# Performance work log

Measured on AMD Instinct MI355X. Metric: run time of the kernel, lower is better.

Reference implementation:

```python
import jax, jax.numpy as jnp
import numpy as np

CHUNK = 32
H = 4

def silu(x):
    return x * jax.nn.sigmoid(x)

def l2norm(x):
    return x * jax.lax.rsqrt(jnp.sum(x * x, -1, keepdims=True) + 1e-6)

def dwconv_causal(x_cl, w):
    # x_cl: (b, C, L), w: (C, k) depthwise causal conv (cross-correlation, left pad k-1)
    k = w.shape[1]
    xp = jnp.pad(x_cl, ((0, 0), (0, 0), (k - 1, 0)))
    return jax.lax.conv_general_dilated(xp, w[:, None, :], (1,), 'VALID',
        dimension_numbers=('NCH', 'OIH', 'NCH'), feature_group_count=x_cl.shape[1])

def short_conv_silu(x_bld, w):
    y = dwconv_causal(jnp.swapaxes(x_bld, 1, 2), w)
    return silu(jnp.swapaxes(y, 1, 2))

def delta_rule_chunkwise(q, k, v, beta, chunk=CHUNK):
    # q,k: (b,h,L,dk)  v: (b,h,L,dv)  beta: (b,h,L)
    b, h, L, dk = q.shape
    dv = v.shape[-1]
    pad = (-L) % chunk
    if pad:
        q, k, v = (jnp.pad(t, ((0, 0), (0, 0), (0, pad), (0, 0))) for t in (q, k, v))
        beta = jnp.pad(beta, ((0, 0), (0, 0), (0, pad)))
    n = (L + pad) // chunk
    q = l2norm(q)
    k = l2norm(k)
    v = v * beta[..., None]
    kb = k * beta[..., None]
    ch = lambda x: x.reshape(b, h, n, chunk, x.shape[-1])
    qc, kc, vc, kbc = map(ch, (q, k, v, kb))
    idx = jnp.arange(chunk)
    strict_lower = (idx[:, None] > idx[None, :]).astype(q.dtype)
    incl_lower = (idx[:, None] >= idx[None, :]).astype(q.dtype)
    # forward substitution to invert (I - tril(beta K K^T, -1)) per chunk
    attn = -jnp.einsum('bhncd,bhned->bhnce', kbc, kc) * strict_lower
    for i in range(1, chunk):
        upd = jnp.einsum('...j,...ji->...i', attn[..., i, :], attn[..., :, :i])
        attn = attn.at[..., i, :i].add(upd)
    attn = attn + jnp.eye(chunk, dtype=q.dtype)
    u = attn @ vc          # (b,h,n,c,dv)
    w = attn @ kbc         # (b,h,n,c,dk)
    xs = tuple(jnp.moveaxis(t, 2, 0) for t in (qc, kc, u, w))
    S0 = jnp.zeros((b, h, dk, dv), q.dtype)
    def step(S, x):
        qi, ki, ui, wi = x
        a_loc = jnp.einsum('bhcd,bhed->bhce', qi, ki) * incl_lower
        ui = ui - wi @ S
        oi = qi @ S + a_loc @ ui
        S = S + jnp.einsum('bhcd,bhcv->bhdv', ki, ui)
        return S, oi
    S, o = jax.lax.scan(step, S0, xs)
    o = jnp.moveaxis(o, 0, 2).reshape(b, h, n * chunk, dv)[:, :, :L]
    return o, S

def multiscale_conv(v, ms_w3, ms_w15, ms_w31, kernel_mix_w, channel_mixer_w):
    # v: (b,l,h,d)
    b, l, h, d = v.shape
    x = jnp.swapaxes(v.reshape(b, l, h * d), 1, 2)  # (b, h*d, l)
    outs = [dwconv_causal(x, w) for w in (ms_w3, ms_w15, ms_w31)]
    y = jnp.concatenate(outs, axis=1)               # (b, 3*h*d, l)
    # faithful to torch rearrange 'b (h kd) l -> b l h kd' on the concat layout
    y = y.reshape(b, h, 3 * d, l).transpose(0, 3, 1, 2)  # (b,l,h,3d)
    y = y @ kernel_mix_w                            # (b,l,h,d)
    y = (y.reshape(b, l, h * d) @ channel_mixer_w).reshape(b, l, h, d)
    return y

def _forward(hidden_states, Wq, Wk, Wv, Wb, conv_q_w, conv_k_w, conv_v_w,
             ms_w3, ms_w15, ms_w31, kernel_mix_w, channel_mixer_w,
             fusion_w1, fusion_b1, fusion_w2, fusion_b2, o_norm_w, Wo):
    b, L, D = hidden_states.shape
    h = H
    dk = Wq.shape[1] // h
    dv = Wv.shape[1] // h
    q = short_conv_silu(hidden_states @ Wq, conv_q_w).reshape(b, L, h, dk)
    k = short_conv_silu(hidden_states @ Wk, conv_k_w).reshape(b, L, h, dk)
    v = short_conv_silu(hidden_states @ Wv, conv_v_w).reshape(b, L, h, dv)
    v_direct = v
    beta = jax.nn.sigmoid(hidden_states @ Wb)  # (b,L,h)
    tr = lambda x: jnp.swapaxes(x, 1, 2)
    delta_out, _S = delta_rule_chunkwise(tr(q), tr(k), tr(v), tr(beta))
    delta_out = jnp.swapaxes(delta_out, 1, 2)  # (b,L,h,dv)
    ms_out = multiscale_conv(v_direct, ms_w3, ms_w15, ms_w31, kernel_mix_w, channel_mixer_w)
    bn = lambda x: jnp.mean(jnp.abs(x), -1)    # (b,L,h)
    gate_features = jnp.concatenate([hidden_states, bn(ms_out), bn(delta_out), bn(v_direct)], -1)
    hdn = jax.nn.gelu(gate_features @ fusion_w1 + fusion_b1, approximate=False)
    logits = (hdn @ fusion_w2 + fusion_b2).reshape(b, L, h, 3)
    wts = jax.nn.softmax(logits, -1)
    o = wts[..., 0:1] * ms_out + wts[..., 1:2] * delta_out + wts[..., 2:3] * v_direct
    o = o * jax.lax.rsqrt(jnp.mean(o * o, -1, keepdims=True) + 1e-5) * o_norm_w  # RMSNorm
    return o.reshape(b, L, h * dv) @ Wo

def setup_inputs() -> dict:
    B, L, D = 4, 2048, 1024
    h, d = H, D // H
    key = jax.random.key(0)
    ks = jax.random.split(key, 20)
    nrm = lambda k, shp, s: (jax.random.normal(k, shp, dtype=jnp.float32) * s)
    inp = {
        'hidden_states': nrm(ks[0], (B, L, D), 1.0),
        'Wq': nrm(ks[1], (D, D), D ** -0.5),
        'Wk': nrm(ks[2], (D, D), D ** -0.5),
        'Wv': nrm(ks[3], (D, D), D ** -0.5),
        'Wb': nrm(ks[4], (D, h), D ** -0.5),
        'conv_q_w': nrm(ks[5], (D, 4), 0.3),
        'conv_k_w': nrm(ks[6], (D, 4), 0.3),
        'conv_v_w': nrm(ks[7], (D, 4), 0.3),
        'ms_w3': nrm(ks[8], (D, 3), 0.02),
        'ms_w15': nrm(ks[9], (D, 15), 0.02),
        'ms_w31': nrm(ks[10], (D, 31), 0.02),
        'kernel_mix_w': nrm(ks[11], (3 * d, d), (3 * d) ** -0.5),
        'channel_mixer_w': nrm(ks[12], (D, D), D ** -0.5),
        'fusion_w1': nrm(ks[13], (D + 3 * h, 2 * D), (D + 3 * h) ** -0.5),
        'fusion_b1': jnp.zeros((2 * D,), jnp.float32),
        'fusion_w2': nrm(ks[14], (2 * D, 3 * h), (2 * D) ** -0.5),
        'fusion_b2': jnp.concatenate([jnp.zeros((2 * h,), jnp.float32), jnp.ones((h,), jnp.float32)]),
        'o_norm_w': jnp.ones((d,), jnp.float32),
        'Wo': nrm(ks[15], (D, D), D ** -0.5),
    }
    return inp

def reference(hidden_states, Wq, Wk, Wv, Wb, conv_q_w, conv_k_w, conv_v_w,
              ms_w3, ms_w15, ms_w31, kernel_mix_w, channel_mixer_w,
              fusion_w1, fusion_b1, fusion_w2, fusion_b2, o_norm_w, Wo):
    return _forward(hidden_states, Wq, Wk, Wv, Wb, conv_q_w, conv_k_w, conv_v_w,
                    ms_w3, ms_w15, ms_w31, kernel_mix_w, channel_mixer_w,
                    fusion_w1, fusion_b1, fusion_w2, fusion_b2, o_norm_w, Wo)
```

## Files before the change

### kernel.cpp

```cpp
#include <hip/hip_runtime.h>
#include <math.h>


typedef __attribute__((ext_vector_type(8))) __bf16 bf16x8;
typedef __attribute__((ext_vector_type(4))) float f32x4;

__device__ inline ushort f2bf(float f) {
    union { float f; unsigned u; } x; x.f = f;
    unsigned u = x.u;
    u += 0x7fffu + ((u >> 16) & 1u);
    return (ushort)(u >> 16);
}
__device__ inline float bf2f(ushort h) {
    union { unsigned u; float f; } x; x.u = ((unsigned)h) << 16;
    return x.f;
}
__device__ inline float ldf(float v) { return v; }
__device__ inline float ldf(ushort v) { return bf2f(v); }

template<int EPI>
__global__ __launch_bounds__(256) void gemm_mfma(
    const ushort* __restrict__ A, const ushort* __restrict__ BT,
    const float* __restrict__ bias, const float* __restrict__ extA,
    const float* __restrict__ extB, void* __restrict__ Cout,
    int M, int N, int K)
{
    __shared__ ushort As[2][128 * 32];
    __shared__ ushort Bs[2][128 * 32];
    __shared__ float bns[(EPI >= 2) ? 128 * 13 : 1];
    __shared__ float exb[(EPI >= 2) ? 12 * 128 : 1];
    const int tid = threadIdx.x;
    const int row0 = blockIdx.y * 128, col0 = blockIdx.x * 128;
    const int lane = tid & 63, wave = tid >> 6;
    const int wr = (wave >> 1) * 64, wc = (wave & 1) * 64;

    if (EPI >= 2) {
        for (int e = tid; e < 128 * 12; e += 256)
            bns[(e / 12) * 13 + (e % 12)] = extA[(long)(row0 + e / 12) * 12 + e % 12];
        for (int e = tid; e < 12 * 128; e += 256)
            exb[e] = extB[(long)(e >> 7) * N + col0 + (e & 127)];
    }

    f32x4 acc[4][4];
    #pragma unroll
    for (int m = 0; m < 4; ++m)
        #pragma unroll
        for (int n = 0; n < 4; ++n) {
            acc[m][n][0] = 0.f; acc[m][n][1] = 0.f;
            acc[m][n][2] = 0.f; acc[m][n][3] = 0.f;
        }

    const int rA = lane & 15;
    const int ko = (lane >> 4) * 8;
    const int srow = tid >> 2;
    const int skk = (tid & 3) * 8;

    for (int k0 = 0; k0 < K; k0 += 64) {
        #pragma unroll
        for (int hf = 0; hf < 2; ++hf) {
            #pragma unroll
            for (int i = 0; i < 2; ++i) {
                const long ga = (long)(row0 + i * 64 + srow) * K + k0 + hf * 32 + skk;
                __builtin_amdgcn_global_load_lds(
                    (const __attribute__((address_space(1))) void*)(A + ga),
                    (__attribute__((address_space(3))) void*)(&As[hf][0] + i * 2048 + wave * 512),
                    16, 0, 0);
                const long gb = (long)(col0 + i * 64 + srow) * K + k0 + hf * 32 + skk;
                __builtin_amdgcn_global_load_lds(
                    (const __attribute__((address_space(1))) void*)(BT + gb),
                    (__attribute__((address_space(3))) void*)(&Bs[hf][0] + i * 2048 + wave * 512),
                    16, 0, 0);
            }
        }
        __syncthreads();
        #pragma unroll
        for (int hf = 0; hf < 2; ++hf) {
            bf16x8 af[4], bfr[4];
            #pragma unroll
            for (int m = 0; m < 4; ++m)
                af[m] = *(const bf16x8*)(&As[hf][0] + (wr + m * 16 + rA) * 32 + ko);
            #pragma unroll
            for (int n = 0; n < 4; ++n)
                bfr[n] = *(const bf16x8*)(&Bs[hf][0] + (wc + n * 16 + rA) * 32 + ko);
            #pragma unroll
            for (int m = 0; m < 4; ++m)
                #pragma unroll
                for (int n = 0; n < 4; ++n)
                    acc[m][n] = __builtin_amdgcn_mfma_f32_16x16x32_bf16(af[m], bfr[n], acc[m][n], 0, 0, 0);
        }
        __syncthreads();
    }

    const int crow = (lane >> 4) * 4;
    const int ccol = lane & 15;
    #pragma unroll
    for (int m = 0; m < 4; ++m) {
        #pragma unroll
        for (int n = 0; n < 4; ++n) {
            #pragma unroll
            for (int r = 0; r < 4; ++r) {
                const int rl = wr + m * 16 + crow + r;
                const int cl = wc + n * 16 + ccol;
                float vv = acc[m][n][r];
                if (EPI >= 2) {
                    vv += bias[col0 + cl];
                    #pragma unroll
                    for (int j = 0; j < 12; ++j) vv += bns[rl * 13 + j] * exb[j * 128 + cl];
                    vv = 0.5f * vv * (1.f + erff(vv * 0.70710678118654752f));
                }
                const long off = (long)(row0 + rl) * N + col0 + cl;
                if (EPI == 0) ((float*)Cout)[off] = vv;
                else ((ushort*)Cout)[off] = f2bf(vv);
            }
        }
    }
}

__global__ __launch_bounds__(256) void transpose_cast(const float* __restrict__ W,
    ushort* __restrict__ WT, int K, int N)
{
    __shared__ float t[32][33];
    const int k0 = blockIdx.y * 32, n0 = blockIdx.x * 32;
    const int c = threadIdx.x & 31, r8 = threadIdx.x >> 5;
    #pragma unroll
    for (int rr = 0; rr < 4; ++rr) {
        const int r = r8 + rr * 8;
        t[r][c] = W[(long)(k0 + r) * N + n0 + c];
    }
    __syncthreads();
    #pragma unroll
    for (int rr = 0; rr < 4; ++rr) {
        const int r = r8 + rr * 8;
        WT[(long)(n0 + r) * K + k0 + c] = f2bf(t[c][r]);
    }
}

__global__ __launch_bounds__(256) void cast_bf16(const float* __restrict__ x,
    ushort* __restrict__ y)
{
    const long i = ((long)blockIdx.x * 256 + threadIdx.x) * 4;
    const float4 v = *(const float4*)(x + i);
    ushort4 o;
    o.x = f2bf(v.x); o.y = f2bf(v.y); o.z = f2bf(v.z); o.w = f2bf(v.w);
    *(ushort4*)(y + i) = o;
}

template<int NOUT, int MODE, typename TA>
__global__ __launch_bounds__(256) void gemm_smallN(const TA* __restrict__ A,
    const float* __restrict__ Bm, const float* __restrict__ bias,
    float* __restrict__ Cm, int K)
{
    __shared__ float part[4][NOUT];
    __shared__ float sm[NOUT];
    const int m = blockIdx.x, tid = threadIdx.x;
    const TA* ar = A + (long)m * K;
    float acc[NOUT];
    #pragma unroll
    for (int j = 0; j < NOUT; ++j) acc[j] = 0.f;
    for (int k = tid; k < K; k += 256) {
        const float a = ldf(ar[k]);
        #pragma unroll
        for (int j = 0; j < NOUT; ++j) acc[j] += a * Bm[(long)k * NOUT + j];
    }
    #pragma unroll
    for (int j = 0; j < NOUT; ++j)
        for (int off = 32; off > 0; off >>= 1) acc[j] += __shfl_down(acc[j], off);
    const int wid = tid >> 6, lane = tid & 63;
    if (lane == 0) {
        #pragma unroll
        for (int j = 0; j < NOUT; ++j) part[wid][j] = acc[j];
    }
    __syncthreads();
    if (tid < NOUT) {
        float s = part[0][tid] + part[1][tid] + part[2][tid] + part[3][tid];
        if (MODE == 0) {
            Cm[(long)m * NOUT + tid] = 1.f / (1.f + expf(-s));
        } else {
            sm[tid] = s + bias[tid];
        }
    }
    if (MODE == 1) {
        __syncthreads();
        if (tid < NOUT) {
            const int hh = tid / 3, r = tid - hh * 3;
            const float a0 = sm[hh * 3], a1 = sm[hh * 3 + 1], a2 = sm[hh * 3 + 2];
            const float mx = fmaxf(a0, fmaxf(a1, a2));
            const float e0 = expf(a0 - mx), e1 = expf(a1 - mx), e2 = expf(a2 - mx);
            const float mine = (r == 0) ? e0 : ((r == 1) ? e1 : e2);
            Cm[(long)m * NOUT + tid] = mine / (e0 + e1 + e2);
        }
    }
}

__global__ __launch_bounds__(256) void conv4_silu(const float* __restrict__ x,
    const float* __restrict__ wc, float* __restrict__ y)
{
    const long idx = (long)blockIdx.x * 256 + threadIdx.x;
    const int c = (int)(idx & 1023);
    const long bl = idx >> 10;
    const int l = (int)(bl & 2047);
    const long b = bl >> 11;
    const float* xp = x + b * 2048 * 1024 + c;
    const float* wp = wc + c * 4;
    float s = 0.f;
    #pragma unroll
    for (int t = 0; t < 4; ++t) {
        const int ll = l - 3 + t;
        if (ll >= 0) s += xp[(long)ll * 1024] * wp[t];
    }
    y[idx] = s / (1.f + expf(-s));
}

__global__ __launch_bounds__(256) void l2norm_bf16(const float* __restrict__ x,
    ushort* __restrict__ y)
{
    const long wid = ((long)blockIdx.x * 256 + threadIdx.x) >> 6;
    const int lane = threadIdx.x & 63;
    const float4 xv = *(const float4*)(x + wid * 256 + lane * 4);
    float ss = xv.x * xv.x + xv.y * xv.y + xv.z * xv.z + xv.w * xv.w;
    for (int off = 32; off > 0; off >>= 1) ss += __shfl_down(ss, off);
    ss = __shfl(ss, 0);
    const float inv = rsqrtf(ss + 1e-6f);
    ushort4 o;
    o.x = f2bf(xv.x * inv); o.y = f2bf(xv.y * inv);
    o.z = f2bf(xv.z * inv); o.w = f2bf(xv.w * inv);
    *(ushort4*)(y + wid * 256 + lane * 4) = o;
}

__global__ __launch_bounds__(256) void chunk_prep(
    const ushort* __restrict__ qn, const ushort* __restrict__ kn,
    const float* __restrict__ v, const float* __restrict__ beta,
    float* __restrict__ u, ushort* __restrict__ w16,
    ushort* __restrict__ kT16, ushort* __restrict__ al16)
{
    __shared__ float kb_s[32 * 256];
    __shared__ float bufB[32 * 256];
    __shared__ float Ms[32 * 33];
    __shared__ float Rs[32 * 33];
    __shared__ float bet[32];
    const int blk = blockIdx.x;
    const int n = blk & 63;
    const int bh = blk >> 6;
    const int h = bh & 3;
    const int b = bh >> 2;
    const int tid = threadIdx.x;
    const long lbase = (long)b * 2048 + n * 32;

    if (tid < 32) bet[tid] = beta[(lbase + tid) * 4 + h];
    __syncthreads();
    for (int e = tid; e < 8192; e += 256) {
        const int c = e >> 8, dd = e & 255;
        const float kv = bf2f(kn[(lbase + c) * 1024 + h * 256 + dd]);
        bufB[dd * 32 + c] = kv;
        kb_s[c * 256 + dd] = kv * bet[c];
    }
    __syncthreads();
    for (int e = tid; e < 8192; e += 256)
        kT16[(long)blk * 8192 + e] = f2bf(bufB[e]);

    const int j = tid & 31, i0 = tid >> 5;
    {
        float m4[4] = {0.f, 0.f, 0.f, 0.f};
        for (int dd = 0; dd < 256; ++dd) {
            const float kt = bufB[dd * 32 + j];
            #pragma unroll
            for (int ii = 0; ii < 4; ++ii) m4[ii] += kb_s[(i0 + 8 * ii) * 256 + dd] * kt;
        }
        #pragma unroll
        for (int ii = 0; ii < 4; ++ii) {
            const int i = i0 + 8 * ii;
            const float mv = (i > j) ? -m4[ii] : 0.f;
            Ms[i * 33 + j] = mv;
            Rs[i * 33 + j] = mv + ((i == j) ? 1.f : 0.f);
        }
    }
    {
        float a4[4] = {0.f, 0.f, 0.f, 0.f};
        for (int dd = 0; dd < 256; ++dd) {
            const float kt = bufB[dd * 32 + j];
            #pragma unroll
            for (int ii = 0; ii < 4; ++ii)
                a4[ii] += bf2f(qn[(lbase + (i0 + 8 * ii)) * 1024 + h * 256 + dd]) * kt;
        }
        #pragma unroll
        for (int ii = 0; ii < 4; ++ii) {
            const int i = i0 + 8 * ii;
            al16[(long)blk * 1024 + i * 32 + j] = f2bf((i >= j) ? a4[ii] : 0.f);
        }
    }
    __syncthreads();
    for (int it = 0; it < 4; ++it) {
        float p4[4] = {0.f, 0.f, 0.f, 0.f};
        for (int kk = 0; kk < 32; ++kk) {
            const float pb = Ms[kk * 33 + j];
            #pragma unroll
            for (int ii = 0; ii < 4; ++ii) p4[ii] += Ms[(i0 + 8 * ii) * 33 + kk] * pb;
        }
        __syncthreads();
        #pragma unroll
        for (int ii = 0; ii < 4; ++ii) Ms[(i0 + 8 * ii) * 33 + j] = p4[ii];
        __syncthreads();
        float r4[4] = {0.f, 0.f, 0.f, 0.f};
        for (int kk = 0; kk < 32; ++kk) {
            const float pb = Ms[kk * 33 + j];
            #pragma unroll
            for (int ii = 0; ii < 4; ++ii) r4[ii] += Rs[(i0 + 8 * ii) * 33 + kk] * pb;
        }
        __syncthreads();
        #pragma unroll
        for (int ii = 0; ii < 4; ++ii) Rs[(i0 + 8 * ii) * 33 + j] += r4[ii];
        __syncthreads();
    }
    for (int e = tid; e < 8192; e += 256) {
        const int c = e >> 8, dd = e & 255;
        bufB[c * 256 + dd] = v[(lbase + c) * 1024 + h * 256 + dd] * bet[c];
    }
    __syncthreads();
    {
        const int dd = tid;
        float accU[32], accW[32];
        #pragma unroll
        for (int r = 0; r < 32; ++r) { accU[r] = 0.f; accW[r] = 0.f; }
        for (int kk = 0; kk < 32; ++kk) {
            const float vv = bufB[kk * 256 + dd];
            const float bb = kb_s[kk * 256 + dd];
            #pragma unroll
            for (int r = 0; r < 32; ++r) {
                const float rr = Rs[r * 33 + kk];
                accU[r] += rr * vv;
                accW[r] += rr * bb;
            }
        }
        const long base = (long)blk * 32;
        #pragma unroll
        for (int r = 0; r < 32; ++r) {
            u  [(base + r) * 256 + dd] = accU[r];
            w16[(base + r) * 256 + dd] = f2bf(accW[r]);
        }
    }
}

__global__ __launch_bounds__(64) void delta_scan_mfma(
    const ushort* __restrict__ q16, const ushort* __restrict__ kT16,
    const ushort* __restrict__ w16, const float* __restrict__ u,
    const ushort* __restrict__ al16, float* __restrict__ dt)
{
    __shared__ __align__(16) ushort Stg[2][25600];
    __shared__ __align__(16) ushort Sb[16 * 264];
    __shared__ __align__(16) ushort Ub[16 * 40];
    const int blk = blockIdx.x;
    const int bh = blk & 15;
    const int sl = blk >> 4;
    const int h = bh & 3;
    const int b = bh >> 2;
    const int v0 = sl * 16;
    const int lane = threadIdx.x;
    const int col = lane & 15;
    const int grp = lane >> 4;
    const int l5 = lane & 31;
    const int lh = lane >> 5;

    f32x4 S[16];
    #pragma unroll
    for (int t = 0; t < 16; ++t) { S[t][0] = 0.f; S[t][1] = 0.f; S[t][2] = 0.f; S[t][3] = 0.f; }
    for (int i = lane; i < 16 * 264; i += 64) Sb[i] = 0;

    const ushort* Wg = w16  + (long)bh * 64 * 8192;
    const ushort* Qg = q16  + ((long)b * 2048) * 1024 + h * 256;
    const ushort* Kg = kT16 + (long)bh * 64 * 8192;
    const ushort* Ag = al16 + (long)bh * 64 * 1024;
    const float*  Ug = u    + (long)bh * 64 * 8192 + grp * 1024 + v0 + col;
    float*        dp = dt   + ((long)b * 2048 + grp * 4) * 1024 + h * 256 + v0 + col;

    auto STAGE = [&](int n, int s) {
        ushort* dst = &Stg[s][0];
        const ushort* wsrc = Wg + (long)n * 8192;
        #pragma unroll
        for (int i = 0; i < 16; ++i) {
            const int row = 2 * i + lh;
            const int key = row & 7;
            __builtin_amdgcn_global_load_lds(
                (const __attribute__((address_space(1))) void*)(wsrc + row * 256 + ((l5 ^ key) << 3)),
                (__attribute__((address_space(3))) void*)(dst + i * 512), 16, 0, 0);
        }
        #pragma unroll
        for (int i = 0; i < 16; ++i) {
            const int row = 2 * i + lh;
            const int key = row & 7;
            __builtin_amdgcn_global_load_lds(
                (const __attribute__((address_space(1))) void*)(Qg + (long)(n * 32 + row) * 1024 + ((l5 ^ key) << 3)),
                (__attribute__((address_space(3))) void*)(dst + 8192 + i * 512), 16, 0, 0);
        }
        const ushort* ksrc = Kg + (long)n * 8192;
        #pragma unroll
        for (int i = 0; i < 16; ++i)
            __builtin_amdgcn_global_load_lds(
                (const __attribute__((address_space(1))) void*)(ksrc + i * 512 + lane * 8),
                (__attribute__((address_space(3))) void*)(dst + 16384 + i * 512), 16, 0, 0);
        const ushort* asrc = Ag + (long)n * 1024;
        #pragma unroll
        for (int i = 0; i < 2; ++i)
            __builtin_amdgcn_global_load_lds(
                (const __attribute__((address_space(1))) void*)(asrc + i * 512 + lane * 8),
                (__attribute__((address_space(3))) void*)(dst + 24576 + i * 512), 16, 0, 0);
    };

    const int xk = (col & 7) << 3;

    STAGE(0, 0);
    float upre[8];
    #pragma unroll
    for (int rt = 0; rt < 2; ++rt)
        #pragma unroll
        for (int r = 0; r < 4; ++r)
            upre[rt * 4 + r] = Ug[rt * 4096 + r * 256];

    for (int n = 0; n < 64; ++n) {
        const int s = n & 1;
        __builtin_amdgcn_sched_barrier(0);
        asm volatile("s_waitcnt vmcnt(8)" ::: "memory");
        __builtin_amdgcn_sched_barrier(0);
        if (n < 63) STAGE(n + 1, s ^ 1);
        __builtin_amdgcn_sched_barrier(0);
        float unext[8];
        {
            const long np = (n < 63) ? (long)(n + 1) : 63;
            #pragma unroll
            for (int rt = 0; rt < 2; ++rt)
                #pragma unroll
                for (int r = 0; r < 4; ++r)
                    unext[rt * 4 + r] = Ug[np * 8192 + rt * 4096 + r * 256];
        }
        __builtin_amdgcn_sched_barrier(0);
        const ushort* Sg = &Stg[s][0];

        bf16x8 sf[8];
        #pragma unroll
        for (int kb = 0; kb < 8; ++kb)
            sf[kb] = *(const bf16x8*)&Sb[col * 264 + kb * 32 + grp * 8];

        f32x4 up[2];
        #pragma unroll
        for (int rt = 0; rt < 2; ++rt) {
            f32x4 a; a[0] = 0.f; a[1] = 0.f; a[2] = 0.f; a[3] = 0.f;
            #pragma unroll
            for (int kb = 0; kb < 8; ++kb) {
                const int widx = ((rt * 16 + col) << 8) + (((kb << 5) + (grp << 3)) ^ xk);
                const bf16x8 wf = *(const bf16x8*)&Sg[widx];
                a = __builtin_amdgcn_mfma_f32_16x16x32_bf16(wf, sf[kb], a, 0, 0, 0);
            }
            #pragma unroll
            for (int r = 0; r < 4; ++r)
                up[rt][r] = upre[rt * 4 + r] - a[r];
        }
        #pragma unroll
        for (int rt = 0; rt < 2; ++rt) {
            ushort4 p;
            p.x = f2bf(up[rt][0]); p.y = f2bf(up[rt][1]);
            p.z = f2bf(up[rt][2]); p.w = f2bf(up[rt][3]);
            *(ushort4*)&Ub[col * 40 + rt * 16 + grp * 4] = p;
        }
        const bf16x8 uf = *(const bf16x8*)&Ub[col * 40 + grp * 8];

        #pragma unroll
        for (int rt = 0; rt < 2; ++rt) {
            f32x4 a; a[0] = 0.f; a[1] = 0.f; a[2] = 0.f; a[3] = 0.f;
            #pragma unroll
            for (int kb = 0; kb < 8; ++kb) {
                const int qidx = 8192 + ((rt * 16 + col) << 8) + (((kb << 5) + (grp << 3)) ^ xk);
                const bf16x8 qf = *(const bf16x8*)&Sg[qidx];
                a = __builtin_amdgcn_mfma_f32_16x16x32_bf16(qf, sf[kb], a, 0, 0, 0);
            }
            const bf16x8 alf = *(const bf16x8*)&Sg[24576 + rt * 512 + col * 32 + grp * 8];
            a = __builtin_amdgcn_mfma_f32_16x16x32_bf16(alf, uf, a, 0, 0, 0);
            #pragma unroll
            for (int r = 0; r < 4; ++r)
                dp[(long)n * 32768 + rt * 16384 + r * 1024] = a[r];
        }

        #pragma unroll
        for (int t = 0; t < 16; ++t) {
            const bf16x8 kf = *(const bf16x8*)&Sg[16384 + t * 512 + col * 32 + grp * 8];
            S[t] = __builtin_amdgcn_mfma_f32_16x16x32_bf16(kf, uf, S[t], 0, 0, 0);
        }

        #pragma unroll
        for (int t = 0; t < 16; ++t) {
            ushort4 p;
            p.x = f2bf(S[t][0]); p.y = f2bf(S[t][1]);
            p.z = f2bf(S[t][2]); p.w = f2bf(S[t][3]);
            *(ushort4*)&Sb[col * 264 + t * 16 + grp * 4] = p;
        }

        #pragma unroll
        for (int i = 0; i < 8; ++i) upre[i] = unext[i];
    }
}

__global__ __launch_bounds__(256) void ms_conv(const float* __restrict__ v,
    const float* __restrict__ w3, const float* __restrict__ w15,
    const float* __restrict__ w31, ushort* __restrict__ y)
{
    const int bid = blockIdx.x;
    const int b = bid >> 10;
    const int oct = (bid >> 2) & 255;
    const int c = ((bid & 3) << 8) + threadIdx.x;
    const int l0 = oct << 3;
    const float* vb = v + ((long)b * 2048) * 1024 + c;
    ushort* yb = y + ((long)b * 2048) * 3072 + c;

    float win[38];
    #pragma unroll
    for (int t = 0; t < 38; ++t) {
        const int ll = l0 - 30 + t;
        win[t] = (ll >= 0) ? vb[(long)ll * 1024] : 0.f;
    }
    {
        float W[31];
        #pragma unroll
        for (int t = 0; t < 31; ++t) W[t] = w31[c * 31 + t];
        #pragma unroll
        for (int j = 0; j < 8; ++j) {
            float s = 0.f;
            #pragma unroll
            for (int t = 0; t < 31; ++t) s += win[j + t] * W[t];
            yb[(long)(l0 + j) * 3072 + 2048] = f2bf(s);
        }
    }
    {
        float W[15];
        #pragma unroll
        for (int t = 0; t < 15; ++t) W[t] = w15[c * 15 + t];
        #pragma unroll
        for (int j = 0; j < 8; ++j) {
            float s = 0.f;
            #pragma unroll
            for (int t = 0; t < 15; ++t) s += win[j + 16 + t] * W[t];
            yb[(long)(l0 + j) * 3072 + 1024] = f2bf(s);
        }
    }
    {
        float W[3];
        #pragma unroll
        for (int t = 0; t < 3; ++t) W[t] = w3[c * 3 + t];
        #pragma unroll
        for (int j = 0; j < 8; ++j) {
            float s = 0.f;
            #pragma unroll
            for (int t = 0; t < 3; ++t) s += win[j + 28 + t] * W[t];
            yb[(long)(l0 + j) * 3072] = f2bf(s);
        }
    }
}

__global__ __launch_bounds__(256) void build_bn(const float* __restrict__ ms,
    const float* __restrict__ dt, const float* __restrict__ v,
    float* __restrict__ bn)
{
    const int bl = blockIdx.x, tid = threadIdx.x;
    const long rb = (long)bl * 1024;
    const int wid = tid >> 6, lane = tid & 63;
    const long base = rb + wid * 256 + lane * 4;
    float* g = bn + (long)bl * 12;
    float4 a;
    float s;
    a = *(const float4*)(ms + base);
    s = fabsf(a.x) + fabsf(a.y) + fabsf(a.z) + fabsf(a.w);
    for (int off = 32; off > 0; off >>= 1) s += __shfl_down(s, off);
    if (lane == 0) g[wid] = s * (1.f / 256.f);
    a = *(const float4*)(dt + base);
    s = fabsf(a.x) + fabsf(a.y) + fabsf(a.z) + fabsf(a.w);
    for (int off = 32; off > 0; off >>= 1) s += __shfl_down(s, off);
    if (lane == 0) g[4 + wid] = s * (1.f / 256.f);
    a = *(const float4*)(v + base);
    s = fabsf(a.x) + fabsf(a.y) + fabsf(a.z) + fabsf(a.w);
    for (int off = 32; off > 0; off >>= 1) s += __shfl_down(s, off);
    if (lane == 0) g[8 + wid] = s * (1.f / 256.f);
}

__global__ __launch_bounds__(256) void blend_rms(const float* __restrict__ ms,
    const float* __restrict__ dt, const float* __restrict__ v,
    const float* __restrict__ wts, const float* __restrict__ onw,
    ushort* __restrict__ o)
{
    const int bl = blockIdx.x, tid = threadIdx.x;
    const int wid = tid >> 6, lane = tid & 63;
    const long base = (long)bl * 1024 + wid * 256 + lane * 4;
    const float* wr = wts + (long)bl * 12 + wid * 3;
    const float w0 = wr[0], w1 = wr[1], w2 = wr[2];
    const float4 m = *(const float4*)(ms + base);
    const float4 d = *(const float4*)(dt + base);
    const float4 x = *(const float4*)(v + base);
    float4 ov;
    ov.x = w0 * m.x + w1 * d.x + w2 * x.x;
    ov.y = w0 * m.y + w1 * d.y + w2 * x.y;
    ov.z = w0 * m.z + w1 * d.z + w2 * x.z;
    ov.w = w0 * m.w + w1 * d.w + w2 * x.w;
    float ss = ov.x * ov.x + ov.y * ov.y + ov.z * ov.z + ov.w * ov.w;
    for (int off = 32; off > 0; off >>= 1) ss += __shfl_down(ss, off);
    ss = __shfl(ss, 0);
    const float inv = rsqrtf(ss * (1.f / 256.f) + 1e-5f);
    const float4 nw = *(const float4*)(onw + lane * 4);
    ushort4 ob;
    ob.x = f2bf(ov.x * inv * nw.x); ob.y = f2bf(ov.y * inv * nw.y);
    ob.z = f2bf(ov.z * inv * nw.z); ob.w = f2bf(ov.w * inv * nw.w);
    *(ushort4*)(o + base) = ob;
}

extern "C" void kernel_launch(void* const* d_in, const int* in_sizes, int n_in,
                              void* d_out, int out_size, void* d_ws, size_t ws_size,
                              hipStream_t stream)
{
    (void)in_sizes; (void)n_in; (void)out_size; (void)ws_size;
    const float* hid   = (const float*)d_in[0];
    const float* Wq    = (const float*)d_in[1];
    const float* Wk    = (const float*)d_in[2];
    const float* Wv    = (const float*)d_in[3];
    const float* Wb    = (const float*)d_in[4];
    const float* cq    = (const float*)d_in[5];
    const float* ck    = (const float*)d_in[6];
    const float* cv    = (const float*)d_in[7];
    const float* w3    = (const float*)d_in[8];
    const float* w15   = (const float*)d_in[9];
    const float* w31   = (const float*)d_in[10];
    const float* kmix  = (const float*)d_in[11];
    const float* cmix  = (const float*)d_in[12];
    const float* fw1   = (const float*)d_in[13];
    const float* fb1   = (const float*)d_in[14];
    const float* fw2   = (const float*)d_in[15];
    const float* fb2   = (const float*)d_in[16];
    const float* onw   = (const float*)d_in[17];
    const float* Wo    = (const float*)d_in[18];
    float* out = (float*)d_out;

    const size_t MiB = 1024 * 1024;
    char* W = (char*)d_ws;
    float*  s0    = (float*)(W);
    char*   s1c   = W + 32 * MiB;
    float*  s1    = (float*)s1c;
    float*  s2    = (float*)(W + 64 * MiB);
    char*   s3    = W + 96 * MiB;
    float*  s4    = (float*)(W + 128 * MiB);
    ushort* hid16 = (ushort*)(W + 160 * MiB);
    ushort* WqT   = (ushort*)(W + 176 * MiB);
    ushort* WkT   = WqT   + 1024 * 1024;
    ushort* WvT   = WkT   + 1024 * 1024;
    ushort* cmixT = WvT   + 1024 * 1024;
    ushort* WoT   = cmixT + 1024 * 1024;
    ushort* fw1T  = WoT   + 1024 * 1024;
    ushort* kmixT = fw1T  + 2048 * 1024;
    float*  beta  = (float*)(W + 191 * MiB);
    ushort* al16  = (ushort*)(W + 191 * MiB + 128 * 1024);
    float*  bnf   = (float*)(W + 193 * MiB + 128 * 1024);
    float*  wts   = bnf + 98304;

    ushort* q16    = (ushort*)s3;
    ushort* k16    = (ushort*)(s3 + 16 * MiB);
    ushort* mix16  = q16;
    ushort* ofin16 = k16;
    ushort* yms16  = (ushort*)s0;
    ushort* hdn16  = (ushort*)s0;
    float*  qlin = s0; float* qtmp = s1;
    float*  u = s0;
    ushort* w16  = (ushort*)s1c;
    ushort* kT16 = (ushort*)(s1c + 16 * MiB);
    float*  dt = s2; float* v = s4; float* msout = s1;

    const dim3 T256(256);
    cast_bf16<<<8192, T256, 0, stream>>>(hid, hid16);
    transpose_cast<<<dim3(32, 32), T256, 0, stream>>>(Wq, WqT, 1024, 1024);
    transpose_cast<<<dim3(32, 32), T256, 0, stream>>>(Wk, WkT, 1024, 1024);
    transpose_cast<<<dim3(32, 32), T256, 0, stream>>>(Wv, WvT, 1024, 1024);
    transpose_cast<<<dim3(32, 32), T256, 0, stream>>>(cmix, cmixT, 1024, 1024);
    transpose_cast<<<dim3(32, 32), T256, 0, stream>>>(Wo, WoT, 1024, 1024);
    transpose_cast<<<dim3(64, 32), T256, 0, stream>>>(fw1, fw1T, 1024, 2048);
    transpose_cast<<<dim3(8, 24), T256, 0, stream>>>(kmix, kmixT, 768, 256);
    gemm_mfma<0><<<dim3(8, 64), T256, 0, stream>>>(hid16, WqT, nullptr, nullptr, nullptr, qlin, 8192, 1024, 1024);
    conv4_silu<<<32768, T256, 0, stream>>>(qlin, cq, qtmp);
    l2norm_bf16<<<8192, T256, 0, stream>>>(qtmp, q16);
    gemm_mfma<0><<<dim3(8, 64), T256, 0, stream>>>(hid16, WkT, nullptr, nullptr, nullptr, qlin, 8192, 1024, 1024);
    conv4_silu<<<32768, T256, 0, stream>>>(qlin, ck, qtmp);
    l2norm_bf16<<<8192, T256, 0, stream>>>(qtmp, k16);
    gemm_mfma<0><<<dim3(8, 64), T256, 0, stream>>>(hid16, WvT, nullptr, nullptr, nullptr, qlin, 8192, 1024, 1024);
    conv4_silu<<<32768, T256, 0, stream>>>(qlin, cv, v);
    gemm_smallN<4, 0><<<8192, T256, 0, stream>>>(hid, Wb, nullptr, beta, 1024);
    chunk_prep<<<1024, T256, 0, stream>>>(q16, k16, v, beta, u, w16, kT16, al16);
    delta_scan_mfma<<<256, dim3(64), 0, stream>>>(q16, kT16, w16, u, al16, dt);
    ms_conv<<<4096, T256, 0, stream>>>(v, w3, w15, w31, yms16);
    gemm_mfma<1><<<dim3(2, 256), T256, 0, stream>>>(yms16, kmixT, nullptr, nullptr, nullptr, mix16, 32768, 256, 768);
    gemm_mfma<0><<<dim3(8, 64), T256, 0, stream>>>(mix16, cmixT, nullptr, nullptr, nullptr, msout, 8192, 1024, 1024);
    build_bn<<<8192, T256, 0, stream>>>(msout, dt, v, bnf);
    gemm_mfma<3><<<dim3(16, 64), T256, 0, stream>>>(hid16, fw1T, fb1, bnf, fw1 + 1024L * 2048, hdn16, 8192, 2048, 1024);
    gemm_smallN<12, 1><<<8192, T256, 0, stream>>>(hdn16, fw2, fb2, wts, 2048);
    blend_rms<<<8192, T256, 0, stream>>>(msout, dt, v, wts, onw, ofin16);
    gemm_mfma<0><<<dim3(8, 64), T256, 0, stream>>>(ofin16, WoT, nullptr, nullptr, nullptr, out, 8192, 1024, 1024);
}
```

Baseline: 837.1 us.

## Load delta-scan operands straight into registers instead of staging through LDS

After: 773.3 us. 1.08x faster.

```diff
diff --git a/kernel.cpp b/kernel.cpp
--- a/kernel.cpp
+++ b/kernel.cpp
@@ -340,12 +340,11 @@
     }
 }
 
-__global__ __launch_bounds__(64) void delta_scan_mfma(
+__global__ __launch_bounds__(64, 1) void delta_scan_mfma(
     const ushort* __restrict__ q16, const ushort* __restrict__ kT16,
     const ushort* __restrict__ w16, const float* __restrict__ u,
     const ushort* __restrict__ al16, float* __restrict__ dt)
 {
-    __shared__ __align__(16) ushort Stg[2][25600];
     __shared__ __align__(16) ushort Sb[16 * 264];
     __shared__ __align__(16) ushort Ub[16 * 40];
     const int blk = blockIdx.x;
@@ -357,58 +356,37 @@
     const int lane = threadIdx.x;
     const int col = lane & 15;
     const int grp = lane >> 4;
-    const int l5 = lane & 31;
-    const int lh = lane >> 5;
+
+    const ushort* wp  = w16  + ((long)bh * 64 * 32 + col) * 256 + grp * 8;
+    const ushort* qp  = q16  + ((long)b * 2048 + col) * 1024 + h * 256 + grp * 8;
+    const ushort* kp  = kT16 + ((long)bh * 64 * 256 + col) * 32 + grp * 8;
+    const ushort* ap  = al16 + ((long)bh * 64 * 32 + col) * 32 + grp * 8;
+    const float*  Ug  = u    + ((long)bh * 64 * 32 + grp * 4) * 256 + v0 + col;
+    float*        dp  = dt   + ((long)b * 2048 + grp * 4) * 1024 + h * 256 + v0 + col;
 
     f32x4 S[16];
     #pragma unroll
     for (int t = 0; t < 16; ++t) { S[t][0] = 0.f; S[t][1] = 0.f; S[t][2] = 0.f; S[t][3] = 0.f; }
-    for (int i = lane; i < 16 * 264; i += 64) Sb[i] = 0;
-
-    const ushort* Wg = w16  + (long)bh * 64 * 8192;
-    const ushort* Qg = q16  + ((long)b * 2048) * 1024 + h * 256;
-    const ushort* Kg = kT16 + (long)bh * 64 * 8192;
-    const ushort* Ag = al16 + (long)bh * 64 * 1024;
-    const float*  Ug = u    + (long)bh * 64 * 8192 + grp * 1024 + v0 + col;
-    float*        dp = dt   + ((long)b * 2048 + grp * 4) * 1024 + h * 256 + v0 + col;
-
-    auto STAGE = [&](int n, int s) {
-        ushort* dst = &Stg[s][0];
-        const ushort* wsrc = Wg + (long)n * 8192;
-        #pragma unroll
-        for (int i = 0; i < 16; ++i) {
-            const int row = 2 * i + lh;
-            const int key = row & 7;
-            __builtin_amdgcn_global_load_lds(
-                (const __attribute__((address_space(1))) void*)(wsrc + row * 256 + ((l5 ^ key) << 3)),
-                (__attribute__((address_space(3))) void*)(dst + i * 512), 16, 0, 0);
-        }
-        #pragma unroll
-        for (int i = 0; i < 16; ++i) {
-            const int row = 2 * i + lh;
-            const int key = row & 7;
-            __builtin_amdgcn_global_load_lds(
-                (const __attribute__((address_space(1))) void*)(Qg + (long)(n * 32 + row) * 1024 + ((l5 ^ key) << 3)),
-                (__attribute__((address_space(3))) void*)(dst + 8192 + i * 512), 16, 0, 0);
-        }
-        const ushort* ksrc = Kg + (long)n * 8192;
-        #pragma unroll
-        for (int i = 0; i < 16; ++i)
-            __builtin_amdgcn_global_load_lds(
-                (const __attribute__((address_space(1))) void*)(ksrc + i * 512 + lane * 8),
-                (__attribute__((address_space(3))) void*)(dst + 16384 + i * 512), 16, 0, 0);
-        const ushort* asrc = Ag + (long)n * 1024;
-        #pragma unroll
-        for (int i = 0; i < 2; ++i)
-            __builtin_amdgcn_global_load_lds(
-                (const __attribute__((address_space(1))) void*)(asrc + i * 512 + lane * 8),
-                (__attribute__((address_space(3))) void*)(dst + 24576 + i * 512), 16, 0, 0);
-    };
-
-    const int xk = (col & 7) << 3;
-
-    STAGE(0, 0);
+
+    bf16x8 wf[2][8], qf[2][8], kf[16], alf[2], sf[8];
     float upre[8];
+
+    #pragma unroll
+    for (int kb = 0; kb < 8; ++kb)
+        #pragma unroll
+        for (int e = 0; e < 8; ++e) sf[kb][e] = (__bf16)0.f;
+
+    #pragma unroll
+    for (int rt = 0; rt < 2; ++rt)
+        #pragma unroll
+        for (int kb = 0; kb < 8; ++kb) {
+            wf[rt][kb] = *(const bf16x8*)(wp + rt * 4096 + kb * 32);
+            qf[rt][kb] = *(const bf16x8*)(qp + (long)rt * 16384 + kb * 32);
+        }
+    #pragma unroll
+    for (int t = 0; t < 16; ++t) kf[t] = *(const bf16x8*)(kp + t * 512);
+    alf[0] = *(const bf16x8*)(ap);
+    alf[1] = *(const bf16x8*)(ap + 512);
     #pragma unroll
     for (int rt = 0; rt < 2; ++rt)
         #pragma unroll
@@ -416,43 +394,25 @@
             upre[rt * 4 + r] = Ug[rt * 4096 + r * 256];
 
     for (int n = 0; n < 64; ++n) {
-        const int s = n & 1;
-        __builtin_amdgcn_sched_barrier(0);
-        asm volatile("s_waitcnt vmcnt(8)" ::: "memory");
-        __builtin_amdgcn_sched_barrier(0);
-        if (n < 63) STAGE(n + 1, s ^ 1);
-        __builtin_amdgcn_sched_barrier(0);
-        float unext[8];
-        {
-            const long np = (n < 63) ? (long)(n + 1) : 63;
+        f32x4 up[2];
+        #pragma unroll
+        for (int rt = 0; rt < 2; ++rt) {
+            f32x4 a; a[0] = 0.f; a[1] = 0.f; a[2] = 0.f; a[3] = 0.f;
+            #pragma unroll
+            for (int kb = 0; kb < 8; ++kb)
+                a = __builtin_amdgcn_mfma_f32_16x16x32_bf16(wf[rt][kb], sf[kb], a, 0, 0, 0);
+            #pragma unroll
+            for (int r = 0; r < 4; ++r)
+                up[rt][r] = upre[rt * 4 + r] - a[r];
+        }
+        if (n < 63) {
             #pragma unroll
             for (int rt = 0; rt < 2; ++rt)
                 #pragma unroll
-                for (int r = 0; r < 4; ++r)
-                    unext[rt * 4 + r] = Ug[np * 8192 + rt * 4096 + r * 256];
-        }
-        __builtin_amdgcn_sched_barrier(0);
-        const ushort* Sg = &Stg[s][0];
-
-        bf16x8 sf[8];
-        #pragma unroll
-        for (int kb = 0; kb < 8; ++kb)
-            sf[kb] = *(const bf16x8*)&Sb[col * 264 + kb * 32 + grp * 8];
-
-        f32x4 up[2];
-        #pragma unroll
-        for (int rt = 0; rt < 2; ++rt) {
-            f32x4 a; a[0] = 0.f; a[1] = 0.f; a[2] = 0.f; a[3] = 0.f;
-            #pragma unroll
-            for (int kb = 0; kb < 8; ++kb) {
-                const int widx = ((rt * 16 + col) << 8) + (((kb << 5) + (grp << 3)) ^ xk);
-                const bf16x8 wf = *(const bf16x8*)&Sg[widx];
-                a = __builtin_amdgcn_mfma_f32_16x16x32_bf16(wf, sf[kb], a, 0, 0, 0);
-            }
-            #pragma unroll
-            for (int r = 0; r < 4; ++r)
-                up[rt][r] = upre[rt * 4 + r] - a[r];
-        }
+                for (int kb = 0; kb < 8; ++kb)
+                    wf[rt][kb] = *(const bf16x8*)(wp + (long)(n + 1) * 8192 + rt * 4096 + kb * 32);
+        }
+
         #pragma unroll
         for (int rt = 0; rt < 2; ++rt) {
             ushort4 p;
@@ -466,22 +426,35 @@
         for (int rt = 0; rt < 2; ++rt) {
             f32x4 a; a[0] = 0.f; a[1] = 0.f; a[2] = 0.f; a[3] = 0.f;
             #pragma unroll
-            for (int kb = 0; kb < 8; ++kb) {
-                const int qidx = 8192 + ((rt * 16 + col) << 8) + (((kb << 5) + (grp << 3)) ^ xk);
-                const bf16x8 qf = *(const bf16x8*)&Sg[qidx];
-                a = __builtin_amdgcn_mfma_f32_16x16x32_bf16(qf, sf[kb], a, 0, 0, 0);
-            }
-            const bf16x8 alf = *(const bf16x8*)&Sg[24576 + rt * 512 + col * 32 + grp * 8];
-            a = __builtin_amdgcn_mfma_f32_16x16x32_bf16(alf, uf, a, 0, 0, 0);
+            for (int kb = 0; kb < 8; ++kb)
+                a = __builtin_amdgcn_mfma_f32_16x16x32_bf16(qf[rt][kb], sf[kb], a, 0, 0, 0);
+            a = __builtin_amdgcn_mfma_f32_16x16x32_bf16(alf[rt], uf, a, 0, 0, 0);
             #pragma unroll
             for (int r = 0; r < 4; ++r)
                 dp[(long)n * 32768 + rt * 16384 + r * 1024] = a[r];
         }
-
-        #pragma unroll
-        for (int t = 0; t < 16; ++t) {
-            const bf16x8 kf = *(const bf16x8*)&Sg[16384 + t * 512 + col * 32 + grp * 8];
-            S[t] = __builtin_amdgcn_mfma_f32_16x16x32_bf16(kf, uf, S[t], 0, 0, 0);
+        if (n < 63) {
+            #pragma unroll
+            for (int rt = 0; rt < 2; ++rt)
+                #pragma unroll
+                for (int kb = 0; kb < 8; ++kb)
+                    qf[rt][kb] = *(const bf16x8*)(qp + (long)(n + 1) * 32768 + (long)rt * 16384 + kb * 32);
+            alf[0] = *(const bf16x8*)(ap + (long)(n + 1) * 1024);
+            alf[1] = *(const bf16x8*)(ap + (long)(n + 1) * 1024 + 512);
+        }
+
+        #pragma unroll
+        for (int t = 0; t < 16; ++t)
+            S[t] = __builtin_amdgcn_mfma_f32_16x16x32_bf16(kf[t], uf, S[t], 0, 0, 0);
+        if (n < 63) {
+            #pragma unroll
+            for (int t = 0; t < 16; ++t)
+                kf[t] = *(const bf16x8*)(kp + (long)(n + 1) * 8192 + t * 512);
+            #pragma unroll
+            for (int rt = 0; rt < 2; ++rt)
+                #pragma unroll
+                for (int r = 0; r < 4; ++r)
+                    upre[rt * 4 + r] = Ug[(long)(n + 1) * 8192 + rt * 4096 + r * 256];
         }
 
         #pragma unroll
@@ -491,9 +464,9 @@
             p.z = f2bf(S[t][2]); p.w = f2bf(S[t][3]);
             *(ushort4*)&Sb[col * 264 + t * 16 + grp * 4] = p;
         }
-
-        #pragma unroll
-        for (int i = 0; i < 8; ++i) upre[i] = unext[i];
+        #pragma unroll
+        for (int kb = 0; kb < 8; ++kb)
+            sf[kb] = *(const bf16x8*)&Sb[col * 264 + kb * 32 + grp * 8];
     }
 }
 
```
